# Kernel optimization log

Measured on AMD Instinct MI355X. Metric: run time of the kernel, lower is better.

## Reference

```python
import jax, jax.numpy as jnp
import numpy as np

B, T, C, H = 8, 2048, 1024, 128  # batch, seq, n_embed, head_size

def setup_inputs() -> dict:
    key = jax.random.key(0)
    ks = jax.random.split(key, 6)
    s = 1.0 / np.sqrt(C)
    return {
        "x": jax.random.normal(ks[0], (B, T, C), dtype=jnp.float32),
        "Wk": jax.random.uniform(ks[1], (C, H), minval=-s, maxval=s, dtype=jnp.float32),
        "Wq": jax.random.uniform(ks[2], (C, H), minval=-s, maxval=s, dtype=jnp.float32),
        "Wv": jax.random.uniform(ks[3], (C, H), minval=-s, maxval=s, dtype=jnp.float32),
        "Wp": jax.random.uniform(ks[4], (H, H), minval=-1/np.sqrt(H), maxval=1/np.sqrt(H), dtype=jnp.float32),
        "bp": jax.random.uniform(ks[5], (H,), minval=-1/np.sqrt(H), maxval=1/np.sqrt(H), dtype=jnp.float32),
    }

def reference(x, Wk, Wq, Wv, Wp, bp):
    # x: [B,T,C]; projections are bias-free
    k = x @ Wk  # [B,T,H]
    q = x @ Wq
    v = x @ Wv
    scale = jnp.asarray(H, x.dtype) ** -0.5
    scores = jnp.einsum('bqh,bkh->bqk', q, k) * scale  # [B,T,T]
    causal = jnp.tril(jnp.ones((T, T), dtype=bool))
    scores = jnp.where(causal, scores, jnp.finfo(x.dtype).min)
    w = jax.nn.softmax(scores, axis=-1)
    out = jnp.einsum('bqk,bkh->bqh', w, v)  # [B,T,H]
    return out @ Wp + bp
```

## Files before the change

### kernel.cpp

```cpp
#include <hip/hip_runtime.h>

constexpr int Bz = 8, Tt = 2048, Cc = 1024, Hh = 128;
constexpr int Mrows = Bz * Tt;
constexpr float kScale = 0.08838834764831843f;

typedef float f32x4 __attribute__((ext_vector_type(4)));
typedef short s16x8 __attribute__((ext_vector_type(8)));
typedef short s16x4 __attribute__((ext_vector_type(4)));
typedef unsigned short u16;

static __device__ __forceinline__ u16 f2bf(float f) {
    union { float f; unsigned int u; } c; c.f = f;
    unsigned int u = c.u;
    unsigned int r = (u + 0x7fffu + ((u >> 16) & 1u)) >> 16;
    return (u16)r;
}
static __device__ __forceinline__ float bf2f(u16 x) {
    union { unsigned int u; float f; } c; c.u = ((unsigned int)x) << 16;
    return c.f;
}

__global__ __launch_bounds__(256) void convw_kernel(
    const float* __restrict__ Wq, const float* __restrict__ Wk,
    const float* __restrict__ Wv, const float* __restrict__ Wp,
    u16* __restrict__ wt, u16* __restrict__ wpt)
{
    int i = blockIdx.x * 256 + threadIdx.x;
    if (i < 393216) {
        int z = i >> 17, r = i & 131071;
        int n = r >> 10, k = r & 1023;
        const float* W = (z == 0) ? Wq : (z == 1) ? Wk : Wv;
        wt[i] = f2bf(W[k * Hh + n]);
    } else {
        int r2 = i - 393216;
        int n = r2 >> 7, k = r2 & 127;
        wpt[r2] = f2bf(Wp[k * Hh + n]);
    }
}

__global__ __launch_bounds__(256, 3)
void qkv_fused(
    const float* __restrict__ x, const u16* __restrict__ wt,
    u16* __restrict__ qo, u16* __restrict__ ko, u16* __restrict__ vt)
{
    __shared__ __align__(16) u16 as[64 * 64];

    const int tid  = threadIdx.x;
    const int m0   = blockIdx.x * 64;
    const int z    = blockIdx.z;
    const int lane = tid & 63, wid = tid >> 6;
    const int l15  = lane & 15, l4 = lane >> 4;
    const int bb   = m0 >> 11;
    const int t0   = m0 & 2047;

    const u16* wz = wt + (size_t)z * 131072;

    f32x4 acc[4][2];
#pragma unroll
    for (int mi = 0; mi < 4; ++mi)
#pragma unroll
        for (int ni = 0; ni < 2; ++ni) {
            f32x4 z4 = {0.f, 0.f, 0.f, 0.f};
            acc[mi][ni] = z4;
        }

    for (int k0 = 0; k0 < Cc; k0 += 64) {
#pragma unroll
        for (int u = 0; u < 4; ++u) {
            int idx = tid + u * 256;
            int m = idx >> 4, kf4 = (idx & 15) * 4;
            float4 xv = *reinterpret_cast<const float4*>(
                &x[(size_t)(m0 + m) * Cc + k0 + kf4]);
            s16x4 bv;
            bv[0] = (short)f2bf(xv.x); bv[1] = (short)f2bf(xv.y);
            bv[2] = (short)f2bf(xv.z); bv[3] = (short)f2bf(xv.w);
            *reinterpret_cast<s16x4*>(&as[m * 64 + (kf4 ^ ((m & 7) << 3))]) = bv;
        }
        s16x8 bfr[2][2];
#pragma unroll
        for (int ni = 0; ni < 2; ++ni) {
            int nloc = wid * 32 + ni * 16 + l15;
            const u16* wb = wz + (size_t)nloc * 1024 + k0;
#pragma unroll
            for (int ks = 0; ks < 2; ++ks)
                bfr[ni][ks] = *reinterpret_cast<const s16x8*>(&wb[ks * 32 + l4 * 8]);
        }
        __syncthreads();

        s16x8 af[4][2];
#pragma unroll
        for (int mi = 0; mi < 4; ++mi) {
            int r = mi * 16 + l15;
#pragma unroll
            for (int ks = 0; ks < 2; ++ks)
                af[mi][ks] = *reinterpret_cast<const s16x8*>(
                    &as[r * 64 + ((ks * 32 + l4 * 8) ^ ((r & 7) << 3))]);
        }
#pragma unroll
        for (int mi = 0; mi < 4; ++mi)
#pragma unroll
            for (int ni = 0; ni < 2; ++ni)
#pragma unroll
                for (int ks = 0; ks < 2; ++ks)
                    acc[mi][ni] = __builtin_amdgcn_mfma_f32_16x16x32_bf16(
                        af[mi][ks], bfr[ni][ks], acc[mi][ni], 0, 0, 0);
        __syncthreads();
    }

#pragma unroll
    for (int mi = 0; mi < 4; ++mi)
#pragma unroll
        for (int ni = 0; ni < 2; ++ni) {
            int colz = wid * 32 + ni * 16 + l15;
            if (z < 2) {
                u16* outp = (z == 0) ? qo : ko;
#pragma unroll
                for (int r = 0; r < 4; ++r) {
                    int row = m0 + mi * 16 + l4 * 4 + r;
                    outp[(size_t)row * Hh + colz] = f2bf(acc[mi][ni][r]);
                }
            } else {
                int trow = t0 + mi * 16 + l4 * 4;
                s16x4 pk;
#pragma unroll
                for (int r = 0; r < 4; ++r) pk[r] = (short)f2bf(acc[mi][ni][r]);
                *reinterpret_cast<s16x4*>(
                    &vt[((size_t)bb * Hh + colz) * Tt + trow]) = pk;
            }
        }
}

template <int LOG>
__global__ __launch_bounds__(256, 4)
void attn_kernel(
    const u16* __restrict__ q, const u16* __restrict__ k,
    const u16* __restrict__ vt,
    u16* __restrict__ Opart, float* __restrict__ Mp, float* __restrict__ Lp)
{
    __shared__ __align__(16) char arena[37888];
    u16* ksl = reinterpret_cast<u16*>(arena);
    u16* vsl = reinterpret_cast<u16*>(arena + 16384);
    u16* psl = reinterpret_cast<u16*>(arena + 32768);
    float* Om  = reinterpret_cast<float*>(arena);
    float* ml2 = reinterpret_cast<float*>(arena + 33792);

    const int NS = 1 << LOG;
    const int tid = threadIdx.x, lane = tid & 63, wid = tid >> 6;
    const int l15 = lane & 15, l4 = lane >> 4;
    const int wq = wid >> 1, half = wid & 1;
    const int bid = blockIdx.x;
    const int b = bid & 7;
    const int rest = bid >> 3;
    const int qt = 63 - (rest >> LOG);
    const int split = rest & (NS - 1);
    const int q0 = qt * 32;
    const int ntf = (qt + 2) >> 1;
    const int lo = (ntf * split) >> LOG;
    const int hi = (ntf * (split + 1)) >> LOG;

    const u16* qb = q  + (size_t)b * Tt * Hh;
    const u16* kb = k  + (size_t)b * Tt * Hh;
    const u16* vb = vt + (size_t)b * Hh * Tt;

    const int qrow = q0 + wq * 16 + l15;
    s16x8 qf[4];
#pragma unroll
    for (int ks = 0; ks < 4; ++ks)
        qf[ks] = *reinterpret_cast<const s16x8*>(
            &qb[(size_t)qrow * Hh + ks * 32 + l4 * 8]);

    f32x4 o[8];
#pragma unroll
    for (int nh = 0; nh < 8; ++nh) { f32x4 z4 = {0.f,0.f,0.f,0.f}; o[nh] = z4; }
    float mreg = -1e30f, lreg = 0.f;

    const int kr_s  = tid >> 2, kc_s = (tid & 3) * 4;
    const int vh_s  = tid >> 1, vc_s = (tid & 1) * 4;
    u16* ps = psl + wid * 640;

    for (int j = lo; j < hi; ++j) {
        const int kv0 = j * 64;

#pragma unroll
        for (int i = 0; i < 4; ++i) {
            s16x8 tk = *reinterpret_cast<const s16x8*>(
                &kb[(size_t)(kv0 + kr_s) * Hh + (kc_s + i) * 8]);
            *reinterpret_cast<s16x8*>(
                &ksl[kr_s * 128 + (((kc_s + i) * 8) ^ ((kr_s & 7) << 3))]) = tk;
        }
#pragma unroll
        for (int i = 0; i < 4; ++i) {
            s16x8 tv = *reinterpret_cast<const s16x8*>(
                &vb[(size_t)vh_s * Tt + kv0 + (vc_s + i) * 8]);
            *reinterpret_cast<s16x8*>(
                &vsl[vh_s * 64 + (((vc_s + i) * 8) ^ ((vh_s & 7) << 3))]) = tv;
        }
        __syncthreads();

        f32x4 sacc[2];
#pragma unroll
        for (int nf = 0; nf < 2; ++nf) { f32x4 z4 = {0.f,0.f,0.f,0.f}; sacc[nf] = z4; }
#pragma unroll
        for (int nf = 0; nf < 2; ++nf) {
            const int kr = half * 32 + nf * 16 + l15;
#pragma unroll
            for (int ks = 0; ks < 4; ++ks) {
                s16x8 kfrag = *reinterpret_cast<const s16x8*>(
                    &ksl[kr * 128 + ((ks * 32 + l4 * 8) ^ ((kr & 7) << 3))]);
                sacc[nf] = __builtin_amdgcn_mfma_f32_16x16x32_bf16(
                    kfrag, qf[ks], sacc[nf], 0, 0, 0);
            }
        }

        const bool diag = (j == ntf - 1);
        float pv2[2][4];
#pragma unroll
        for (int nf = 0; nf < 2; ++nf)
#pragma unroll
            for (int r = 0; r < 4; ++r) {
                float s = sacc[nf][r] * kScale;
                if (diag) {
                    int kvg = kv0 + half * 32 + nf * 16 + l4 * 4 + r;
                    if (kvg > qrow) s = -1e30f;
                }
                pv2[nf][r] = s;
            }
        float mx = fmaxf(fmaxf(fmaxf(pv2[0][0], pv2[0][1]), fmaxf(pv2[0][2], pv2[0][3])),
                         fmaxf(fmaxf(pv2[1][0], pv2[1][1]), fmaxf(pv2[1][2], pv2[1][3])));
        mx = fmaxf(mx, __shfl_xor(mx, 16));
        mx = fmaxf(mx, __shfl_xor(mx, 32));
        const float mold = mreg;
        const float mnew = fmaxf(mold, mx);
        const float scl = __expf(mold - mnew);
        mreg = mnew;
        float rs = 0.f;
#pragma unroll
        for (int nf = 0; nf < 2; ++nf)
#pragma unroll
            for (int r = 0; r < 4; ++r) {
                float pp = __expf(pv2[nf][r] - mnew);
                pv2[nf][r] = pp; rs += pp;
            }
        rs += __shfl_xor(rs, 16);
        rs += __shfl_xor(rs, 32);
        lreg = lreg * scl + rs;

        if (!__all(mold == mnew)) {
            float sclr[4];
#pragma unroll
            for (int r = 0; r < 4; ++r) sclr[r] = __shfl(scl, l4 * 4 + r);
#pragma unroll
            for (int nh = 0; nh < 8; ++nh)
#pragma unroll
                for (int r = 0; r < 4; ++r) o[nh][r] *= sclr[r];
        }

#pragma unroll
        for (int nf = 0; nf < 2; ++nf) {
            s16x4 pk4;
#pragma unroll
            for (int r = 0; r < 4; ++r) pk4[r] = (short)f2bf(pv2[nf][r]);
            *reinterpret_cast<s16x4*>(&ps[l15 * 40 + nf * 16 + l4 * 4]) = pk4;
        }
        s16x8 pa = *reinterpret_cast<const s16x8*>(&ps[l15 * 40 + l4 * 8]);

#pragma unroll
        for (int nh = 0; nh < 8; ++nh) {
            const int hr = nh * 16 + l15;
            s16x8 vfrag = *reinterpret_cast<const s16x8*>(
                &vsl[hr * 64 + ((half * 32 + l4 * 8) ^ ((hr & 7) << 3))]);
            o[nh] = __builtin_amdgcn_mfma_f32_16x16x32_bf16(
                pa, vfrag, o[nh], 0, 0, 0);
        }
        __syncthreads();
    }

#pragma unroll
    for (int nh = 0; nh < 8; ++nh)
#pragma unroll
        for (int r = 0; r < 4; ++r)
            Om[((wid * 16) + l4 * 4 + r) * 132 + nh * 16 + l15] = o[nh][r];
    if (lane < 16) {
        ml2[wid * 32 + lane] = mreg;
        ml2[wid * 32 + 16 + lane] = lreg;
    }
    __syncthreads();

    {
        const int row = tid >> 3, ch = tid & 7;
        const int rg = row >> 4, r16 = row & 15;
        const int w0 = rg * 2, w1 = rg * 2 + 1;
        float m0v = ml2[w0 * 32 + r16], m1v = ml2[w1 * 32 + r16];
        float M = fmaxf(m0v, m1v);
        float f0 = __expf(m0v - M), f1 = __expf(m1v - M);
        float L = f0 * ml2[w0 * 32 + 16 + r16] + f1 * ml2[w1 * 32 + 16 + r16];
        const size_t gm = (size_t)b * Tt + q0 + row;
        union { u16 u[8]; s16x8 v; } pk0, pk1;
#pragma unroll
        for (int c = 0; c < 8; ++c) {
            float a = f0 * Om[(w0 * 16 + r16) * 132 + ch * 16 + c]
                    + f1 * Om[(w1 * 16 + r16) * 132 + ch * 16 + c];
            pk0.u[c] = f2bf(a);
        }
#pragma unroll
        for (int c = 0; c < 8; ++c) {
            float a = f0 * Om[(w0 * 16 + r16) * 132 + ch * 16 + 8 + c]
                    + f1 * Om[(w1 * 16 + r16) * 132 + ch * 16 + 8 + c];
            pk1.u[c] = f2bf(a);
        }
        u16* op = Opart + ((size_t)split * Mrows + gm) * 128 + ch * 16;
        *reinterpret_cast<s16x8*>(op) = pk0.v;
        *reinterpret_cast<s16x8*>(op + 8) = pk1.v;
        if (ch == 0) {
            Mp[split * Mrows + gm] = M;
            Lp[split * Mrows + gm] = L;
        }
    }
}

template <int NS>
__global__ __launch_bounds__(256) void merge_proj(
    const u16* __restrict__ Opart, const float* __restrict__ Mp,
    const float* __restrict__ Lp, const u16* __restrict__ wpt,
    const float* __restrict__ bp, float* __restrict__ O)
{
    __shared__ __align__(16) u16 pm[32 * 136];
    __shared__ float fs[NS][32], invs[32];

    const int tid = threadIdx.x, lane = tid & 63, wid = tid >> 6;
    const int l15 = lane & 15, l4 = lane >> 4;
    const int m0r = blockIdx.x * 32;

    if (tid < 32) {
        float M = -1e30f;
#pragma unroll
        for (int w = 0; w < NS; ++w)
            M = fmaxf(M, Mp[(size_t)w * Mrows + m0r + tid]);
        float L = 0.f;
#pragma unroll
        for (int w = 0; w < NS; ++w) {
            float a = __expf(Mp[(size_t)w * Mrows + m0r + tid] - M);
            fs[w][tid] = a;
            L += a * Lp[(size_t)w * Mrows + m0r + tid];
        }
        invs[tid] = 1.f / L;
    }
    __syncthreads();

#pragma unroll
    for (int u = 0; u < 2; ++u) {
        int idx = tid + u * 256;
        int row = idx >> 4, g = idx & 15;
        const size_t base = (size_t)(m0r + row) * 128 + g * 8;
        float acc8[8];
#pragma unroll
        for (int c = 0; c < 8; ++c) acc8[c] = 0.f;
#pragma unroll
        for (int w = 0; w < NS; ++w) {
            s16x8 p = *reinterpret_cast<const s16x8*>(
                &Opart[(size_t)w * Mrows * 128 + base]);
            float a = fs[w][row];
#pragma unroll
            for (int c = 0; c < 8; ++c) acc8[c] += a * bf2f((u16)p[c]);
        }
        float inv = invs[row];
        union { u16 u[8]; s16x8 v; } pk;
#pragma unroll
        for (int c = 0; c < 8; ++c) pk.u[c] = f2bf(acc8[c] * inv);
        *reinterpret_cast<s16x8*>(&pm[row * 136 + g * 8]) = pk.v;
    }
    __syncthreads();

    {
        const int rg2 = (wid & 1) * 16;
        const int cg  = (wid >> 1) * 64;
        const int row2 = rg2 + l15;
        s16x8 af2[4];
#pragma unroll
        for (int ks = 0; ks < 4; ++ks)
            af2[ks] = *reinterpret_cast<const s16x8*>(
                &pm[row2 * 136 + ks * 32 + l4 * 8]);
#pragma unroll
        for (int ng = 0; ng < 4; ++ng) {
            const int ncol = cg + ng * 16 + l15;
            f32x4 pacc = {0.f, 0.f, 0.f, 0.f};
#pragma unroll
            for (int ks = 0; ks < 4; ++ks) {
                s16x8 wf = *reinterpret_cast<const s16x8*>(
                    &wpt[(size_t)ncol * 128 + ks * 32 + l4 * 8]);
                pacc = __builtin_amdgcn_mfma_f32_16x16x32_bf16(
                    af2[ks], wf, pacc, 0, 0, 0);
            }
            float bias = bp[ncol];
#pragma unroll
            for (int r = 0; r < 4; ++r)
                O[(size_t)(m0r + rg2 + l4 * 4 + r) * Hh + ncol] =
                    pacc[r] + bias;
        }
    }
}

extern "C" void kernel_launch(void* const* d_in, const int* in_sizes, int n_in,
                              void* d_out, int out_size, void* d_ws, size_t ws_size,
                              hipStream_t stream) {
    const float* x  = (const float*)d_in[0];
    const float* Wk = (const float*)d_in[1];
    const float* Wq = (const float*)d_in[2];
    const float* Wv = (const float*)d_in[3];
    const float* Wp = (const float*)d_in[4];
    const float* bp = (const float*)d_in[5];
    float* out = (float*)d_out;

    u16* wtb = (u16*)d_ws;
    u16* wpt = wtb + 393216;
    u16* qw  = wpt + 16384;
    u16* kw  = qw + (size_t)Mrows * Hh;
    u16* vtb = kw + (size_t)Mrows * Hh;
    u16* opart = vtb + (size_t)Mrows * Hh;

    const size_t head = ((size_t)409600 + 3u * Mrows * Hh) * 2;
    const size_t need4 = head + (size_t)4 * Mrows * Hh * 2 + (size_t)2 * 4 * Mrows * 4;
    const bool use4 = (ws_size >= need4);
    const int ns = use4 ? 4 : 2;

    float* Mpart = (float*)(opart + (size_t)ns * Mrows * Hh);
    float* Lpart = Mpart + (size_t)ns * Mrows;

    convw_kernel<<<1600, 256, 0, stream>>>(Wq, Wk, Wv, Wp, wtb, wpt);
    qkv_fused<<<dim3(Mrows / 64, 1, 3), 256, 0, stream>>>(x, wtb, qw, kw, vtb);
    if (use4) {
        attn_kernel<2><<<64 * 4 * 8, 256, 0, stream>>>(qw, kw, vtb, opart, Mpart, Lpart);
        merge_proj<4><<<Mrows / 32, 256, 0, stream>>>(opart, Mpart, Lpart, wpt, bp, out);
    } else {
        attn_kernel<1><<<64 * 2 * 8, 256, 0, stream>>>(qw, kw, vtb, opart, Mpart, Lpart);
        merge_proj<2><<<Mrows / 32, 256, 0, stream>>>(opart, Mpart, Lpart, wpt, bp, out);
    }
}
```

Measured before the change: 80.25 us.

## Load x directly into MFMA fragments in QKV projection, drop LDS staging

```diff
diff --git a/kernel.cpp b/kernel.cpp
--- a/kernel.cpp
+++ b/kernel.cpp
@@ -18,6 +18,16 @@
 static __device__ __forceinline__ float bf2f(u16 x) {
     union { unsigned int u; float f; } c; c.u = ((unsigned int)x) << 16;
     return c.f;
+}
+
+static __device__ __forceinline__ s16x8 pack_bf8(f32x4 a, f32x4 b) {
+    union { unsigned int u[4]; s16x8 v; } o;
+    union { float f; unsigned int u; } c0, c1;
+    c0.f = a[0]; c1.f = a[1]; o.u[0] = __byte_perm(c0.u, c1.u, 0x7632);
+    c0.f = a[2]; c1.f = a[3]; o.u[1] = __byte_perm(c0.u, c1.u, 0x7632);
+    c0.f = b[0]; c1.f = b[1]; o.u[2] = __byte_perm(c0.u, c1.u, 0x7632);
+    c0.f = b[2]; c1.f = b[3]; o.u[3] = __byte_perm(c0.u, c1.u, 0x7632);
+    return o.v;
 }
 
 __global__ __launch_bounds__(256) void convw_kernel(
@@ -38,15 +48,13 @@
     }
 }
 
-__global__ __launch_bounds__(256, 3)
+__global__ __launch_bounds__(256)
 void qkv_fused(
     const float* __restrict__ x, const u16* __restrict__ wt,
     u16* __restrict__ qo, u16* __restrict__ ko, u16* __restrict__ vt)
 {
-    __shared__ __align__(16) u16 as[64 * 64];
-
     const int tid  = threadIdx.x;
-    const int m0   = blockIdx.x * 64;
+    const int m0   = blockIdx.x * 32;
     const int z    = blockIdx.z;
     const int lane = tid & 63, wid = tid >> 6;
     const int l15  = lane & 15, l4 = lane >> 4;
@@ -55,9 +63,14 @@
 
     const u16* wz = wt + (size_t)z * 131072;
 
-    f32x4 acc[4][2];
-#pragma unroll
-    for (int mi = 0; mi < 4; ++mi)
+    const float* xr0 = &x[(size_t)(m0 + l15) * Cc + l4 * 8];
+    const float* xr1 = xr0 + (size_t)16 * Cc;
+    const u16*   wb0 = wz + (size_t)(wid * 32 + l15) * 1024 + l4 * 8;
+    const u16*   wb1 = wb0 + (size_t)16 * 1024;
+
+    f32x4 acc[2][2];
+#pragma unroll
+    for (int mi = 0; mi < 2; ++mi)
 #pragma unroll
         for (int ni = 0; ni < 2; ++ni) {
             f32x4 z4 = {0.f, 0.f, 0.f, 0.f};
@@ -65,50 +78,35 @@
         }
 
     for (int k0 = 0; k0 < Cc; k0 += 64) {
-#pragma unroll
-        for (int u = 0; u < 4; ++u) {
-            int idx = tid + u * 256;
-            int m = idx >> 4, kf4 = (idx & 15) * 4;
-            float4 xv = *reinterpret_cast<const float4*>(
-                &x[(size_t)(m0 + m) * Cc + k0 + kf4]);
-            s16x4 bv;
-            bv[0] = (short)f2bf(xv.x); bv[1] = (short)f2bf(xv.y);
-            bv[2] = (short)f2bf(xv.z); bv[3] = (short)f2bf(xv.w);
-            *reinterpret_cast<s16x4*>(&as[m * 64 + (kf4 ^ ((m & 7) << 3))]) = bv;
+        s16x8 af[2][2];
+#pragma unroll
+        for (int ks = 0; ks < 2; ++ks) {
+            int ko_ = k0 + ks * 32;
+            f32x4 a0 = *reinterpret_cast<const f32x4*>(xr0 + ko_);
+            f32x4 a1 = *reinterpret_cast<const f32x4*>(xr0 + ko_ + 4);
+            f32x4 b0 = *reinterpret_cast<const f32x4*>(xr1 + ko_);
+            f32x4 b1 = *reinterpret_cast<const f32x4*>(xr1 + ko_ + 4);
+            af[0][ks] = pack_bf8(a0, a1);
+            af[1][ks] = pack_bf8(b0, b1);
         }
         s16x8 bfr[2][2];
 #pragma unroll
-        for (int ni = 0; ni < 2; ++ni) {
-            int nloc = wid * 32 + ni * 16 + l15;
-            const u16* wb = wz + (size_t)nloc * 1024 + k0;
-#pragma unroll
-            for (int ks = 0; ks < 2; ++ks)
-                bfr[ni][ks] = *reinterpret_cast<const s16x8*>(&wb[ks * 32 + l4 * 8]);
-        }
-        __syncthreads();
-
-        s16x8 af[4][2];
-#pragma unroll
-        for (int mi = 0; mi < 4; ++mi) {
-            int r = mi * 16 + l15;
-#pragma unroll
-            for (int ks = 0; ks < 2; ++ks)
-                af[mi][ks] = *reinterpret_cast<const s16x8*>(
-                    &as[r * 64 + ((ks * 32 + l4 * 8) ^ ((r & 7) << 3))]);
-        }
-#pragma unroll
-        for (int mi = 0; mi < 4; ++mi)
+        for (int ks = 0; ks < 2; ++ks) {
+            bfr[0][ks] = *reinterpret_cast<const s16x8*>(wb0 + k0 + ks * 32);
+            bfr[1][ks] = *reinterpret_cast<const s16x8*>(wb1 + k0 + ks * 32);
+        }
+#pragma unroll
+        for (int mi = 0; mi < 2; ++mi)
 #pragma unroll
             for (int ni = 0; ni < 2; ++ni)
 #pragma unroll
                 for (int ks = 0; ks < 2; ++ks)
                     acc[mi][ni] = __builtin_amdgcn_mfma_f32_16x16x32_bf16(
                         af[mi][ks], bfr[ni][ks], acc[mi][ni], 0, 0, 0);
-        __syncthreads();
-    }
-
-#pragma unroll
-    for (int mi = 0; mi < 4; ++mi)
+    }
+
+#pragma unroll
+    for (int mi = 0; mi < 2; ++mi)
 #pragma unroll
         for (int ni = 0; ni < 2; ++ni) {
             int colz = wid * 32 + ni * 16 + l15;
@@ -427,7 +425,7 @@
     float* Lpart = Mpart + (size_t)ns * Mrows;
 
     convw_kernel<<<1600, 256, 0, stream>>>(Wq, Wk, Wv, Wp, wtb, wpt);
-    qkv_fused<<<dim3(Mrows / 64, 1, 3), 256, 0, stream>>>(x, wtb, qw, kw, vtb);
+    qkv_fused<<<dim3(Mrows / 32, 1, 3), 256, 0, stream>>>(x, wtb, qw, kw, vtb);
     if (use4) {
         attn_kernel<2><<<64 * 4 * 8, 256, 0, stream>>>(qw, kw, vtb, opart, Mpart, Lpart);
         merge_proj<4><<<Mrows / 32, 256, 0, stream>>>(opart, Mpart, Lpart, wpt, bp, out);
```

New measurement: 175.5 us. +118.7%, slower.
